# Kernel tuning notes

Measured on AMD Instinct MI355X. Metric: run time of the kernel, lower is better.

## Reference

```python
import jax, jax.numpy as jnp
import numpy as np

N = 50000      # nodes
E = 800000     # edges (avg degree 16)
F_IN = 64      # node_features
HID = 64       # hidden_dim
OUT = 32       # output_dim


def setup_inputs() -> dict:
    key = jax.random.key(0)
    ks = jax.random.split(key, 24)
    inp = {
        "x": jax.random.normal(ks[0], (N, F_IN), jnp.float32),
        "edge_index": jax.random.randint(ks[1], (2, E), 0, N, dtype=jnp.int64),
        "edge_weight": jax.random.uniform(ks[2], (E,), jnp.float32),
    }
    def w(k, i, o):
        return jax.random.normal(k, (i, o), jnp.float32) * 0.05
    ki = 3
    # 6 ChebConv (K=2) weight pairs + bias: gates z, r, h for x-path and h-path
    for nm in ["xz", "hz", "xr", "hr", "xh", "hh"]:
        din = F_IN if nm[0] == "x" else HID
        inp[f"W{nm}0"] = w(ks[ki], din, HID); ki += 1
        inp[f"W{nm}1"] = w(ks[ki], din, HID); ki += 1
        inp[f"b{nm}"] = jnp.zeros((HID,), jnp.float32)
    inp["Wlin"] = w(ks[ki], HID, OUT); ki += 1
    inp["blin"] = jnp.zeros((OUT,), jnp.float32)
    return inp


def reference(x, edge_index, edge_weight,
              Wxz0, Wxz1, bxz, Whz0, Whz1, bhz,
              Wxr0, Wxr1, bxr, Whr0, Whr1, bhr,
              Wxh0, Wxh1, bxh, Whh0, Whh1, bhh,
              Wlin, blin):
    src, dst = edge_index[0], edge_index[1]
    # scaled Chebyshev Laplacian (lambda_max=2, sym norm): L_hat = -D^{-1/2} A D^{-1/2}, diag 0
    deg = jax.ops.segment_sum(edge_weight, src, num_segments=N)
    deg_safe = jnp.where(deg > 0, deg, 1.0)
    dinv = jnp.where(deg > 0, jax.lax.rsqrt(deg_safe), 0.0)
    norm = -dinv[src] * edge_weight * dinv[dst]  # [E]

    def prop(v):  # L_hat @ v via gather-scatter
        return jax.ops.segment_sum(norm[:, None] * v[src], dst, num_segments=N)

    def cheb(v, W0, W1, b):  # ChebConv K=2: T0(v) W0 + T1(v) W1 + b
        return v @ W0 + prop(v) @ W1 + b

    H = jnp.zeros((N, HID), x.dtype)  # GConvGRU initial state
    Z = jax.nn.sigmoid(cheb(x, Wxz0, Wxz1, bxz) + cheb(H, Whz0, Whz1, bhz))
    R = jax.nn.sigmoid(cheb(x, Wxr0, Wxr1, bxr) + cheb(H, Whr0, Whr1, bhr))
    Ht = jnp.tanh(cheb(x, Wxh0, Wxh1, bxh) + cheb(H * R, Whh0, Whh1, bhh))
    H = Z * H + (1.0 - Z) * Ht

    h = H @ Wlin + blin
    # F.normalize(p=2, dim=1)
    return h / jnp.maximum(jnp.linalg.norm(h, axis=1, keepdims=True), 1e-12)
```

## Files before the change

kernel.cpp:

```cpp
#include <hip/hip_runtime.h>
#include <math.h>

#define N_NODES 50000
#define F 64
#define OUTF 32
#define NX4 (N_NODES * 16)
#define NPREP (16384 + 2048 + 128 + 32)
#define CAP 64

#define HCHUNK 64
#define HR 25000

#define HC2 32
#define SPL 8
#define HR2 6250

typedef __bf16 v8bf __attribute__((ext_vector_type(8)));
typedef float v4f __attribute__((ext_vector_type(4)));

static __device__ __forceinline__ unsigned short f2bf(float f) {
    union { float f; unsigned u; } v; v.f = f;
    unsigned r = v.u + 0x7FFFu + ((v.u >> 16) & 1u);
    return (unsigned short)(r >> 16);
}
static __device__ __forceinline__ float bf2f(unsigned short h) {
    union { unsigned u; float f; } v; v.u = ((unsigned)h) << 16;
    return v.f;
}

__global__ void pre_kernel(const float4* __restrict__ x4, uint2* __restrict__ xb4,
                           const float* __restrict__ Wxz0, const float* __restrict__ Wxz1,
                           const float* __restrict__ Wxh0, const float* __restrict__ Wxh1,
                           const float* __restrict__ Wlin,
                           const float* __restrict__ bxz, const float* __restrict__ bhz,
                           const float* __restrict__ bxh, const float* __restrict__ bhh,
                           const float* __restrict__ blin,
                           unsigned short* __restrict__ Bt, unsigned short* __restrict__ Wlt,
                           float* __restrict__ bzc, float* __restrict__ blc) {
    int i = blockIdx.x * 256 + threadIdx.x;
    if (i < NX4) {
        float4 v = x4[i];
        uint2 o;
        o.x = (unsigned)f2bf(v.x) | ((unsigned)f2bf(v.y) << 16);
        o.y = (unsigned)f2bf(v.z) | ((unsigned)f2bf(v.w) << 16);
        xb4[i] = o;
    } else {
        int idx = i - NX4;
        if (idx < 16384) {
            int k = idx & 127, n = idx >> 7;
            float v;
            if (k < 64) v = (n < 64) ? Wxz0[k * 64 + n] : Wxh0[k * 64 + (n - 64)];
            else        v = (n < 64) ? Wxz1[(k - 64) * 64 + n] : Wxh1[(k - 64) * 64 + (n - 64)];
            Bt[n * 128 + k] = f2bf(v);
        } else if (idx < 16384 + 2048) {
            int j = idx - 16384; int k = j & 63, n = j >> 6;
            Wlt[n * 64 + k] = f2bf(Wlin[k * 32 + n]);
        } else if (idx < 16384 + 2048 + 128) {
            int j = idx - 16384 - 2048;
            bzc[j] = (j < 64) ? (bxz[j] + bhz[j]) : (bxh[j - 64] + bhh[j - 64]);
        } else if (idx < NPREP) {
            int j = idx - 16384 - 2048 - 128;
            blc[j] = blin[j];
        }
    }
}

__launch_bounds__(1024)
__global__ void hist_kernel(const int* __restrict__ src, const float* __restrict__ ew,
                            const int* __restrict__ dst,
                            float* __restrict__ partW, unsigned* __restrict__ partC, int E) {
    __shared__ float sdeg[HR];
    int b = blockIdx.x, tid = threadIdx.x;
    if (b < 128) {
        int chunk = b >> 1, half = b & 1;
        int nbase = half * HR;
        int epb = (E + HCHUNK - 1) / HCHUNK;
        int lo = chunk * epb, hi = min(lo + epb, E);
        for (int i = tid; i < HR; i += 1024) sdeg[i] = 0.f;
        __syncthreads();
        for (int e = lo + tid; e < hi; e += 1024) {
            int s = src[e];
            unsigned ls = (unsigned)(s - nbase);
            if (ls < HR) atomicAdd(&sdeg[ls], ew[e]);
        }
        __syncthreads();
        for (int i = tid; i < HR; i += 1024)
            partW[(size_t)chunk * N_NODES + nbase + i] = sdeg[i];
    } else {
        unsigned* cnt = (unsigned*)sdeg;
        int b2 = b - 128;
        int chunk = b2 >> 3, split = b2 & 7;
        int nbase = split * HR2;
        int epb = (E + HC2 - 1) / HC2;
        int lo = chunk * epb, hi = min(lo + epb, E);
        for (int i = tid; i < HR2; i += 1024) cnt[i] = 0u;
        __syncthreads();
        for (int e = lo + tid; e < hi; e += 1024) {
            unsigned ls = (unsigned)(dst[e] - nbase);
            if (ls < HR2) atomicAdd(&cnt[ls], 1u);
        }
        __syncthreads();
        for (int i = tid; i < HR2; i += 1024)
            partC[(size_t)chunk * N_NODES + nbase + i] = cnt[i];
    }
}

__global__ void reducew_kernel(const float* __restrict__ partW, unsigned* __restrict__ partC,
                               float* __restrict__ dinv, unsigned* __restrict__ cursor) {
    int i = blockIdx.x * 256 + threadIdx.x;
    if (i >= N_NODES) return;
    float s = 0.f;
    #pragma unroll
    for (int b = 0; b < HCHUNK; ++b) s += partW[(size_t)b * N_NODES + i];
    dinv[i] = s > 0.f ? rsqrtf(s) : 0.f;
    unsigned run = 0u;
    #pragma unroll
    for (int c = 0; c < HC2; ++c) {
        unsigned v = partC[(size_t)c * N_NODES + i];
        partC[(size_t)c * N_NODES + i] = run;
        run += v;
    }
    cursor[i] = run;
}

__launch_bounds__(1024)
__global__ void place_kernel(const int* __restrict__ src, const int* __restrict__ dst,
                             const float* __restrict__ w, const float* __restrict__ dinv,
                             const unsigned* __restrict__ offs, unsigned* __restrict__ rec, int E) {
    __shared__ unsigned curs[HR2];
    int b = blockIdx.x, tid = threadIdx.x;
    int chunk = b >> 3, split = b & 7;
    int nbase = split * HR2;
    for (int i = tid; i < HR2; i += 1024)
        curs[i] = offs[(size_t)chunk * N_NODES + nbase + i];
    __syncthreads();
    int epb = (E + HC2 - 1) / HC2;
    int lo = chunk * epb, hi = min(lo + epb, E);
    for (int e = lo + tid; e < hi; e += 1024) {
        int d = dst[e];
        unsigned ls = (unsigned)(d - nbase);
        if (ls < HR2) {
            int s = src[e];
            float coef = -dinv[s] * w[e] * dinv[d];
            unsigned pos = atomicAdd(&curs[ls], 1u);
            if (pos < CAP)
                rec[((size_t)d << 6) + pos] = (unsigned)s | ((unsigned)f2bf(coef) << 16);
        }
    }
}

__launch_bounds__(256)
__global__ void accum_kernel(const unsigned* __restrict__ rec, const unsigned* __restrict__ cursor,
                             const unsigned short* __restrict__ xb, unsigned short* __restrict__ Pb) {
    int n = blockIdx.x * 4 + (threadIdx.x >> 6);
    int lane = threadIdx.x & 63;
    int cnt = min((int)cursor[n], CAP);
    unsigned r = (lane < cnt) ? rec[((size_t)n << 6) + lane] : 0u;
    float acc = 0.f;
    for (int j = 0; j < cnt; j += 8) {
        unsigned rv[8]; float xv[8];
        #pragma unroll
        for (int t = 0; t < 8; ++t) rv[t] = __shfl(r, j + t);
        #pragma unroll
        for (int t = 0; t < 8; ++t) xv[t] = bf2f(xb[(size_t)(rv[t] & 0xFFFFu) * 64 + lane]);
        #pragma unroll
        for (int t = 0; t < 8; ++t) acc = fmaf(bf2f((unsigned short)(rv[t] >> 16)), xv[t], acc);
    }
    Pb[(size_t)n * 64 + lane] = f2bf(acc);
}

__launch_bounds__(256, 2)
__global__ void dense_kernel(const unsigned short* __restrict__ xb, const unsigned short* __restrict__ Pb,
                             const unsigned short* __restrict__ Bt, const unsigned short* __restrict__ Wlt,
                             const float* __restrict__ bzc, const float* __restrict__ blc,
                             float* __restrict__ out) {
    __shared__ unsigned short Bs[128 * 136];
    __shared__ unsigned short Wls[32 * 80];
    __shared__ unsigned short Hs[4][16 * 80];
    __shared__ float bzs[128], bls[32];

    int tid = threadIdx.x;
    for (int c = tid; c < 4096; c += 256) {
        int n = c >> 5; int k4 = (c & 31) * 4;
        *(uint2*)&Bs[n * 136 + k4] = *(const uint2*)&Bt[n * 128 + k4];
    }
    for (int c = tid; c < 512; c += 256) {
        int n = c >> 4; int k4 = (c & 15) * 4;
        *(uint2*)&Wls[n * 80 + k4] = *(const uint2*)&Wlt[n * 64 + k4];
    }
    if (tid < 128) bzs[tid] = bzc[tid];
    if (tid < 32) bls[tid] = blc[tid];
    __syncthreads();

    int wv = tid >> 6, lane = tid & 63;
    int nl = lane & 15, q = lane >> 4;
    int ngroups = (N_NODES + 63) / 64;

    for (int g = blockIdx.x; g < ngroups; g += gridDim.x) {
        int rowbase = g * 64 + wv * 16;
        int arow = rowbase + nl; if (arow >= N_NODES) arow = N_NODES - 1;

        v4f acc[8];
        #pragma unroll
        for (int i = 0; i < 8; ++i) acc[i] = (v4f)(0.f);

        #pragma unroll
        for (int kk = 0; kk < 4; ++kk) {
            int k0 = kk * 32 + q * 8;
            const unsigned short* ap = (kk < 2) ? (xb + (size_t)arow * 64 + k0)
                                                : (Pb + (size_t)arow * 64 + (k0 - 64));
            v8bf a = *(const v8bf*)ap;
            #pragma unroll
            for (int tn = 0; tn < 8; ++tn) {
                v8bf b = *(const v8bf*)&Bs[(tn * 16 + nl) * 136 + kk * 32 + q * 8];
                acc[tn] = __builtin_amdgcn_mfma_f32_16x16x32_bf16(a, b, acc[tn], 0, 0, 0);
            }
        }

        #pragma unroll
        for (int tn = 0; tn < 4; ++tn) {
            int n = tn * 16 + nl;
            float bz = bzs[n], bh = bzs[64 + n];
            #pragma unroll
            for (int r = 0; r < 4; ++r) {
                float z = acc[tn][r] + bz;
                float h = acc[tn + 4][r] + bh;
                float sg = 1.f / (1.f + __expf(-z));
                float th = 1.f - 2.f / (__expf(2.f * h) + 1.f);
                int m = q * 4 + r;
                Hs[wv][m * 80 + n] = f2bf((1.f - sg) * th);
            }
        }

        v4f acc2[2];
        acc2[0] = (v4f)(0.f); acc2[1] = (v4f)(0.f);
        #pragma unroll
        for (int kk = 0; kk < 2; ++kk) {
            v8bf a = *(const v8bf*)&Hs[wv][nl * 80 + kk * 32 + q * 8];
            #pragma unroll
            for (int tn = 0; tn < 2; ++tn) {
                v8bf b = *(const v8bf*)&Wls[(tn * 16 + nl) * 80 + kk * 32 + q * 8];
                acc2[tn] = __builtin_amdgcn_mfma_f32_16x16x32_bf16(a, b, acc2[tn], 0, 0, 0);
            }
        }

        float o0[4], o1[4];
        #pragma unroll
        for (int r = 0; r < 4; ++r) {
            o0[r] = acc2[0][r] + bls[nl];
            o1[r] = acc2[1][r] + bls[16 + nl];
        }
        #pragma unroll
        for (int r = 0; r < 4; ++r) {
            float ss = o0[r] * o0[r] + o1[r] * o1[r];
            ss += __shfl_xor(ss, 1);
            ss += __shfl_xor(ss, 2);
            ss += __shfl_xor(ss, 4);
            ss += __shfl_xor(ss, 8);
            float dn = fmaxf(sqrtf(ss), 1e-12f);
            int node = rowbase + q * 4 + r;
            if (node < N_NODES) {
                out[node * 32 + nl] = o0[r] / dn;
                out[node * 32 + 16 + nl] = o1[r] / dn;
            }
        }
    }
}

extern "C" void kernel_launch(void* const* d_in, const int* in_sizes, int n_in,
                              void* d_out, int out_size, void* d_ws, size_t ws_size,
                              hipStream_t stream) {
    const float* x    = (const float*)d_in[0];
    const int*   ei   = (const int*)d_in[1];
    const float* ew   = (const float*)d_in[2];
    const float* Wxz0 = (const float*)d_in[3];
    const float* Wxz1 = (const float*)d_in[4];
    const float* bxz  = (const float*)d_in[5];
    const float* bhz  = (const float*)d_in[8];
    const float* Wxh0 = (const float*)d_in[15];
    const float* Wxh1 = (const float*)d_in[16];
    const float* bxh  = (const float*)d_in[17];
    const float* bhh  = (const float*)d_in[20];
    const float* Wlin = (const float*)d_in[21];
    const float* blin = (const float*)d_in[22];
    float* out = (float*)d_out;

    int E = in_sizes[2];
    const int* src = ei;
    const int* dst = ei + E;

    char* base = (char*)d_ws;
    float*          dinv   = (float*)(base + 0);
    unsigned short* xb     = (unsigned short*)(base + 200000);
    unsigned*       partC  = (unsigned*)(base + 6600000);
    unsigned short* Pb     = (unsigned short*)(base + 6600000);
    float*          partW  = (float*)(base + 13000000);
    unsigned*       rec    = (unsigned*)(base + 13000000);
    char* p = base + 25800000;
    unsigned short* Bt     = (unsigned short*)p;      p += 128 * 128 * 2;
    unsigned short* Wlt    = (unsigned short*)p;      p += 32 * 64 * 2;
    float*          bzc    = (float*)p;               p += 128 * 4;
    float*          blc    = (float*)p;
    unsigned*       cursor = (unsigned*)(base + 25840000);

    pre_kernel<<<(NX4 + NPREP + 255) / 256, 256, 0, stream>>>(
        (const float4*)x, (uint2*)xb,
        Wxz0, Wxz1, Wxh0, Wxh1, Wlin, bxz, bhz, bxh, bhh, blin,
        Bt, Wlt, bzc, blc);

    hist_kernel<<<128 + HC2 * SPL, 1024, 0, stream>>>(src, ew, dst, partW, partC, E);

    reducew_kernel<<<(N_NODES + 255) / 256, 256, 0, stream>>>(partW, partC, dinv, cursor);

    place_kernel<<<HC2 * SPL, 1024, 0, stream>>>(src, dst, ew, dinv, partC, rec, E);

    accum_kernel<<<N_NODES / 4, 256, 0, stream>>>(rec, cursor, xb, Pb);

    dense_kernel<<<512, 256, 0, stream>>>(xb, Pb, Bt, Wlt, bzc, blc, out);
}
```

Measured before the change: 200.0 us.

## Fuse preprocessing into histogram kernel, pack counts as u16, fold SpMM into dense GEMM

Merges the bf16 conversion and weight prep into the histogram kernel, and packs the per-chunk destination counts and cursors as 16-bit halves of shared-memory words. This lets each block cover twice as many nodes, so 64 chunks fit with 4 splits. The sparse aggregation from the old accum kernel now runs inside the dense kernel, writing each row group's propagated features to LDS so the Pb round trip through global memory and one launch disappear. The catch is lower parallelism for the gather, since it now runs in 512 persistent blocks with a serial 16-row loop per wave. It also adds more shared memory per block and relies on 16-bit counts not overflowing.

```diff
diff --git a/kernel.cpp b/kernel.cpp
--- a/kernel.cpp
+++ b/kernel.cpp
@@ -8,12 +8,11 @@
 #define NPREP (16384 + 2048 + 128 + 32)
 #define CAP 64
 
-#define HCHUNK 64
-#define HR 25000
-
-#define HC2 32
-#define SPL 8
-#define HR2 6250
+#define CH 64
+#define WHALF 25000
+#define CSPL 4
+#define CR 12500
+#define CRW 6250
 
 typedef __bf16 v8bf __attribute__((ext_vector_type(8)));
 typedef float v4f __attribute__((ext_vector_type(4)));
@@ -28,96 +27,97 @@
     return v.f;
 }
 
-__global__ void pre_kernel(const float4* __restrict__ x4, uint2* __restrict__ xb4,
-                           const float* __restrict__ Wxz0, const float* __restrict__ Wxz1,
-                           const float* __restrict__ Wxh0, const float* __restrict__ Wxh1,
-                           const float* __restrict__ Wlin,
-                           const float* __restrict__ bxz, const float* __restrict__ bhz,
-                           const float* __restrict__ bxh, const float* __restrict__ bhh,
-                           const float* __restrict__ blin,
-                           unsigned short* __restrict__ Bt, unsigned short* __restrict__ Wlt,
-                           float* __restrict__ bzc, float* __restrict__ blc) {
-    int i = blockIdx.x * 256 + threadIdx.x;
-    if (i < NX4) {
-        float4 v = x4[i];
-        uint2 o;
-        o.x = (unsigned)f2bf(v.x) | ((unsigned)f2bf(v.y) << 16);
-        o.y = (unsigned)f2bf(v.z) | ((unsigned)f2bf(v.w) << 16);
-        xb4[i] = o;
-    } else {
-        int idx = i - NX4;
-        if (idx < 16384) {
-            int k = idx & 127, n = idx >> 7;
-            float v;
-            if (k < 64) v = (n < 64) ? Wxz0[k * 64 + n] : Wxh0[k * 64 + (n - 64)];
-            else        v = (n < 64) ? Wxz1[(k - 64) * 64 + n] : Wxh1[(k - 64) * 64 + (n - 64)];
-            Bt[n * 128 + k] = f2bf(v);
-        } else if (idx < 16384 + 2048) {
-            int j = idx - 16384; int k = j & 63, n = j >> 6;
-            Wlt[n * 64 + k] = f2bf(Wlin[k * 32 + n]);
-        } else if (idx < 16384 + 2048 + 128) {
-            int j = idx - 16384 - 2048;
-            bzc[j] = (j < 64) ? (bxz[j] + bhz[j]) : (bxh[j - 64] + bhh[j - 64]);
-        } else if (idx < NPREP) {
-            int j = idx - 16384 - 2048 - 128;
-            blc[j] = blin[j];
-        }
-    }
-}
-
 __launch_bounds__(1024)
-__global__ void hist_kernel(const int* __restrict__ src, const float* __restrict__ ew,
-                            const int* __restrict__ dst,
-                            float* __restrict__ partW, unsigned* __restrict__ partC, int E) {
-    __shared__ float sdeg[HR];
-    int b = blockIdx.x, tid = threadIdx.x;
+__global__ void prehist_kernel(const float4* __restrict__ x4, uint2* __restrict__ xb4,
+                               const int* __restrict__ src, const int* __restrict__ dst,
+                               const float* __restrict__ ew,
+                               const float* __restrict__ Wxz0, const float* __restrict__ Wxz1,
+                               const float* __restrict__ Wxh0, const float* __restrict__ Wxh1,
+                               const float* __restrict__ Wlin,
+                               const float* __restrict__ bxz, const float* __restrict__ bhz,
+                               const float* __restrict__ bxh, const float* __restrict__ bhh,
+                               const float* __restrict__ blin,
+                               unsigned short* __restrict__ Bt, unsigned short* __restrict__ Wlt,
+                               float* __restrict__ bzc, float* __restrict__ blc,
+                               float* __restrict__ partW, unsigned short* __restrict__ partC,
+                               int E) {
+    __shared__ float smf[WHALF];
+    unsigned* smu = (unsigned*)smf;
+    int tid = threadIdx.x, b = blockIdx.x;
+
+    for (int i = b * 1024 + tid; i < NX4 + NPREP; i += 384 * 1024) {
+        if (i < NX4) {
+            float4 v = x4[i];
+            uint2 o;
+            o.x = (unsigned)f2bf(v.x) | ((unsigned)f2bf(v.y) << 16);
+            o.y = (unsigned)f2bf(v.z) | ((unsigned)f2bf(v.w) << 16);
+            xb4[i] = o;
+        } else {
+            int idx = i - NX4;
+            if (idx < 16384) {
+                int k = idx & 127, n = idx >> 7;
+                float v;
+                if (k < 64) v = (n < 64) ? Wxz0[k * 64 + n] : Wxh0[k * 64 + (n - 64)];
+                else        v = (n < 64) ? Wxz1[(k - 64) * 64 + n] : Wxh1[(k - 64) * 64 + (n - 64)];
+                Bt[n * 128 + k] = f2bf(v);
+            } else if (idx < 16384 + 2048) {
+                int j = idx - 16384; int k = j & 63, n = j >> 6;
+                Wlt[n * 64 + k] = f2bf(Wlin[k * 32 + n]);
+            } else if (idx < 16384 + 2048 + 128) {
+                int j = idx - 16384 - 2048;
+                bzc[j] = (j < 64) ? (bxz[j] + bhz[j]) : (bxh[j - 64] + bhh[j - 64]);
+            } else if (idx < NPREP) {
+                int j = idx - 16384 - 2048 - 128;
+                blc[j] = blin[j];
+            }
+        }
+    }
+
+    int epb = (E + CH - 1) / CH;
     if (b < 128) {
         int chunk = b >> 1, half = b & 1;
-        int nbase = half * HR;
-        int epb = (E + HCHUNK - 1) / HCHUNK;
+        int nbase = half * WHALF;
         int lo = chunk * epb, hi = min(lo + epb, E);
-        for (int i = tid; i < HR; i += 1024) sdeg[i] = 0.f;
+        for (int i = tid; i < WHALF; i += 1024) smf[i] = 0.f;
         __syncthreads();
         for (int e = lo + tid; e < hi; e += 1024) {
             int s = src[e];
             unsigned ls = (unsigned)(s - nbase);
-            if (ls < HR) atomicAdd(&sdeg[ls], ew[e]);
+            if (ls < WHALF) atomicAdd(&smf[ls], ew[e]);
         }
         __syncthreads();
-        for (int i = tid; i < HR; i += 1024)
-            partW[(size_t)chunk * N_NODES + nbase + i] = sdeg[i];
+        for (int i = tid; i < WHALF; i += 1024)
+            partW[(size_t)chunk * N_NODES + nbase + i] = smf[i];
     } else {
-        unsigned* cnt = (unsigned*)sdeg;
         int b2 = b - 128;
-        int chunk = b2 >> 3, split = b2 & 7;
-        int nbase = split * HR2;
-        int epb = (E + HC2 - 1) / HC2;
+        int chunk = b2 >> 2, split = b2 & 3;
+        int nbase = split * CR;
         int lo = chunk * epb, hi = min(lo + epb, E);
-        for (int i = tid; i < HR2; i += 1024) cnt[i] = 0u;
+        for (int i = tid; i < CRW; i += 1024) smu[i] = 0u;
         __syncthreads();
         for (int e = lo + tid; e < hi; e += 1024) {
             unsigned ls = (unsigned)(dst[e] - nbase);
-            if (ls < HR2) atomicAdd(&cnt[ls], 1u);
+            if (ls < CR) atomicAdd(&smu[ls >> 1], 1u << ((ls & 1) << 4));
         }
         __syncthreads();
-        for (int i = tid; i < HR2; i += 1024)
-            partC[(size_t)chunk * N_NODES + nbase + i] = cnt[i];
-    }
-}
-
-__global__ void reducew_kernel(const float* __restrict__ partW, unsigned* __restrict__ partC,
+        unsigned* pc32 = (unsigned*)partC + (((size_t)chunk * N_NODES + nbase) >> 1);
+        for (int i = tid; i < CRW; i += 1024) pc32[i] = smu[i];
+    }
+}
+
+__global__ void reducew_kernel(const float* __restrict__ partW, unsigned short* __restrict__ partC,
                                float* __restrict__ dinv, unsigned* __restrict__ cursor) {
     int i = blockIdx.x * 256 + threadIdx.x;
     if (i >= N_NODES) return;
     float s = 0.f;
     #pragma unroll
-    for (int b = 0; b < HCHUNK; ++b) s += partW[(size_t)b * N_NODES + i];
+    for (int c = 0; c < CH; ++c) s += partW[(size_t)c * N_NODES + i];
     dinv[i] = s > 0.f ? rsqrtf(s) : 0.f;
     unsigned run = 0u;
     #pragma unroll
-    for (int c = 0; c < HC2; ++c) {
+    for (int c = 0; c < CH; ++c) {
         unsigned v = partC[(size_t)c * N_NODES + i];
-        partC[(size_t)c * N_NODES + i] = run;
+        partC[(size_t)c * N_NODES + i] = (unsigned short)run;
         run += v;
     }
     cursor[i] = run;
@@ -126,57 +126,41 @@
 __launch_bounds__(1024)
 __global__ void place_kernel(const int* __restrict__ src, const int* __restrict__ dst,
                              const float* __restrict__ w, const float* __restrict__ dinv,
-                             const unsigned* __restrict__ offs, unsigned* __restrict__ rec, int E) {
-    __shared__ unsigned curs[HR2];
+                             const unsigned short* __restrict__ offs, unsigned* __restrict__ rec, int E) {
+    __shared__ unsigned curs[CRW];
     int b = blockIdx.x, tid = threadIdx.x;
-    int chunk = b >> 3, split = b & 7;
-    int nbase = split * HR2;
-    for (int i = tid; i < HR2; i += 1024)
-        curs[i] = offs[(size_t)chunk * N_NODES + nbase + i];
+    int chunk = b >> 2, split = b & 3;
+    int nbase = split * CR;
+    const unsigned* offs32 = (const unsigned*)offs + (((size_t)chunk * N_NODES + nbase) >> 1);
+    for (int i = tid; i < CRW; i += 1024) curs[i] = offs32[i];
     __syncthreads();
-    int epb = (E + HC2 - 1) / HC2;
+    int epb = (E + CH - 1) / CH;
     int lo = chunk * epb, hi = min(lo + epb, E);
     for (int e = lo + tid; e < hi; e += 1024) {
         int d = dst[e];
         unsigned ls = (unsigned)(d - nbase);
-        if (ls < HR2) {
+        if (ls < CR) {
             int s = src[e];
             float coef = -dinv[s] * w[e] * dinv[d];
-            unsigned pos = atomicAdd(&curs[ls], 1u);
+            unsigned sh = (ls & 1) << 4;
+            unsigned old = atomicAdd(&curs[ls >> 1], 1u << sh);
+            unsigned pos = (old >> sh) & 0xFFFFu;
             if (pos < CAP)
                 rec[((size_t)d << 6) + pos] = (unsigned)s | ((unsigned)f2bf(coef) << 16);
         }
     }
 }
 
-__launch_bounds__(256)
-__global__ void accum_kernel(const unsigned* __restrict__ rec, const unsigned* __restrict__ cursor,
-                             const unsigned short* __restrict__ xb, unsigned short* __restrict__ Pb) {
-    int n = blockIdx.x * 4 + (threadIdx.x >> 6);
-    int lane = threadIdx.x & 63;
-    int cnt = min((int)cursor[n], CAP);
-    unsigned r = (lane < cnt) ? rec[((size_t)n << 6) + lane] : 0u;
-    float acc = 0.f;
-    for (int j = 0; j < cnt; j += 8) {
-        unsigned rv[8]; float xv[8];
-        #pragma unroll
-        for (int t = 0; t < 8; ++t) rv[t] = __shfl(r, j + t);
-        #pragma unroll
-        for (int t = 0; t < 8; ++t) xv[t] = bf2f(xb[(size_t)(rv[t] & 0xFFFFu) * 64 + lane]);
-        #pragma unroll
-        for (int t = 0; t < 8; ++t) acc = fmaf(bf2f((unsigned short)(rv[t] >> 16)), xv[t], acc);
-    }
-    Pb[(size_t)n * 64 + lane] = f2bf(acc);
-}
-
 __launch_bounds__(256, 2)
-__global__ void dense_kernel(const unsigned short* __restrict__ xb, const unsigned short* __restrict__ Pb,
+__global__ void dense_kernel(const unsigned short* __restrict__ xb,
+                             const unsigned* __restrict__ rec, const unsigned* __restrict__ cursor,
                              const unsigned short* __restrict__ Bt, const unsigned short* __restrict__ Wlt,
                              const float* __restrict__ bzc, const float* __restrict__ blc,
                              float* __restrict__ out) {
     __shared__ unsigned short Bs[128 * 136];
     __shared__ unsigned short Wls[32 * 80];
     __shared__ unsigned short Hs[4][16 * 80];
+    __shared__ unsigned short Ps[4][16 * 80];
     __shared__ float bzs[128], bls[32];
 
     int tid = threadIdx.x;
@@ -200,6 +184,26 @@
         int rowbase = g * 64 + wv * 16;
         int arow = rowbase + nl; if (arow >= N_NODES) arow = N_NODES - 1;
 
+        #pragma unroll 2
+        for (int m = 0; m < 16; ++m) {
+            int n = rowbase + m;
+            float acc = 0.f;
+            if (n < N_NODES) {
+                int cnt = min((int)cursor[n], CAP);
+                unsigned r = (lane < cnt) ? rec[((size_t)n << 6) + lane] : 0u;
+                for (int j = 0; j < cnt; j += 8) {
+                    unsigned rv[8]; float xv[8];
+                    #pragma unroll
+                    for (int t = 0; t < 8; ++t) rv[t] = __shfl(r, j + t);
+                    #pragma unroll
+                    for (int t = 0; t < 8; ++t) xv[t] = bf2f(xb[(size_t)(rv[t] & 0xFFFFu) * 64 + lane]);
+                    #pragma unroll
+                    for (int t = 0; t < 8; ++t) acc = fmaf(bf2f((unsigned short)(rv[t] >> 16)), xv[t], acc);
+                }
+            }
+            Ps[wv][m * 80 + lane] = f2bf(acc);
+        }
+
         v4f acc[8];
         #pragma unroll
         for (int i = 0; i < 8; ++i) acc[i] = (v4f)(0.f);
@@ -207,9 +211,9 @@
         #pragma unroll
         for (int kk = 0; kk < 4; ++kk) {
             int k0 = kk * 32 + q * 8;
-            const unsigned short* ap = (kk < 2) ? (xb + (size_t)arow * 64 + k0)
-                                                : (Pb + (size_t)arow * 64 + (k0 - 64));
-            v8bf a = *(const v8bf*)ap;
+            v8bf a;
+            if (kk < 2) a = *(const v8bf*)(xb + (size_t)arow * 64 + k0);
+            else        a = *(const v8bf*)&Ps[wv][nl * 80 + (k0 - 64)];
             #pragma unroll
             for (int tn = 0; tn < 8; ++tn) {
                 v8bf b = *(const v8bf*)&Bs[(tn * 16 + nl) * 136 + kk * 32 + q * 8];
@@ -292,29 +296,24 @@
     char* base = (char*)d_ws;
     float*          dinv   = (float*)(base + 0);
     unsigned short* xb     = (unsigned short*)(base + 200000);
-    unsigned*       partC  = (unsigned*)(base + 6600000);
-    unsigned short* Pb     = (unsigned short*)(base + 6600000);
-    float*          partW  = (float*)(base + 13000000);
-    unsigned*       rec    = (unsigned*)(base + 13000000);
-    char* p = base + 25800000;
+    float*          partW  = (float*)(base + 6600000);
+    unsigned short* partC  = (unsigned short*)(base + 19400000);
+    unsigned*       rec    = (unsigned*)(base + 25800000);
+    char* p = base + 38600000;
     unsigned short* Bt     = (unsigned short*)p;      p += 128 * 128 * 2;
     unsigned short* Wlt    = (unsigned short*)p;      p += 32 * 64 * 2;
     float*          bzc    = (float*)p;               p += 128 * 4;
     float*          blc    = (float*)p;
-    unsigned*       cursor = (unsigned*)(base + 25840000);
-
-    pre_kernel<<<(NX4 + NPREP + 255) / 256, 256, 0, stream>>>(
-        (const float4*)x, (uint2*)xb,
+    unsigned*       cursor = (unsigned*)(base + 38700000);
+
+    prehist_kernel<<<384, 1024, 0, stream>>>(
+        (const float4*)x, (uint2*)xb, src, dst, ew,
         Wxz0, Wxz1, Wxh0, Wxh1, Wlin, bxz, bhz, bxh, bhh, blin,
-        Bt, Wlt, bzc, blc);
-
-    hist_kernel<<<128 + HC2 * SPL, 1024, 0, stream>>>(src, ew, dst, partW, partC, E);
+        Bt, Wlt, bzc, blc, partW, partC, E);
 
     reducew_kernel<<<(N_NODES + 255) / 256, 256, 0, stream>>>(partW, partC, dinv, cursor);
 
-    place_kernel<<<HC2 * SPL, 1024, 0, stream>>>(src, dst, ew, dinv, partC, rec, E);
-
-    accum_kernel<<<N_NODES / 4, 256, 0, stream>>>(rec, cursor, xb, Pb);
-
-    dense_kernel<<<512, 256, 0, stream>>>(xb, Pb, Bt, Wlt, bzc, blc, out);
-}
+    place_kernel<<<CH * CSPL, 1024, 0, stream>>>(src, dst, ew, dinv, partC, rec, E);
+
+    dense_kernel<<<512, 256, 0, stream>>>(xb, rec, cursor, Bt, Wlt, bzc, blc, out);
+}
```

New measurement: 216.3 us. 8.1% more time.
